# Kernel optimization log

Hardware: AMD Instinct MI355X
Metric: run time of the kernel (lower is better)

Reference implementation:

```python
import jax, jax.numpy as jnp
import numpy as np

HEADS = 4
DIM_HEAD = 64
MAP_SIZE = 16
SCALE = DIM_HEAD ** (-0.5)


def _split_heads(x):
    # torch rearrange 'b (dim_head heads) h w -> b heads (h w) dim_head'
    B, C, H, W = x.shape
    x = x.reshape(B, DIM_HEAD, HEADS, H * W)
    return jnp.transpose(x, (0, 2, 3, 1))  # [B, heads, N, dim_head]


def _merge_heads(x, H, W):
    # torch rearrange 'b heads (h w) dim_head -> b (dim_head heads) h w'
    B, h, N, d = x.shape
    return jnp.transpose(x, (0, 3, 1, 2)).reshape(B, d * h, H, W)


def setup_inputs() -> dict:
    key = jax.random.key(0)
    ks = jax.random.split(key, 6)
    feat = jax.random.normal(ks[0], (4, 256, 96, 96), jnp.float32)
    semantic_map = jax.random.normal(ks[1], (4, 256, 16, 16), jnp.float32)
    # 1x1 conv weights, shape [out_ch, in_ch]; scaled like fan-in init
    W_feat_qv = 0.05 * jax.random.normal(ks[2], (512, 256), jnp.float32)
    W_map_qv = 0.05 * jax.random.normal(ks[3], (512, 256), jnp.float32)
    W_feat_out = 0.05 * jax.random.normal(ks[4], (256, 256), jnp.float32)
    W_map_out = 0.05 * jax.random.normal(ks[5], (256, 256), jnp.float32)
    return {
        "feat": feat,
        "semantic_map": semantic_map,
        "W_feat_qv": W_feat_qv,
        "W_map_qv": W_map_qv,
        "W_feat_out": W_feat_out,
        "W_map_out": W_map_out,
    }


def reference(feat, semantic_map, W_feat_qv, W_map_qv, W_feat_out, W_map_out):
    B, C, H, W = feat.shape
    # 1x1 convs == per-pixel channel matmuls
    fqv = jnp.einsum("oc,bchw->bohw", W_feat_qv, feat)
    feat_q, feat_v = jnp.split(fqv, 2, axis=1)
    mqv = jnp.einsum("oc,bchw->bohw", W_map_qv, semantic_map)
    map_q, map_v = jnp.split(mqv, 2, axis=1)

    feat_q, feat_v = _split_heads(feat_q), _split_heads(feat_v)  # [B,h,N,d]
    map_q, map_v = _split_heads(map_q), _split_heads(map_v)      # [B,h,M,d]

    attn = jnp.einsum("bhid,bhjd->bhij", feat_q, map_q) * SCALE  # [B,h,N,M]
    feat_map_attn = jax.nn.softmax(attn, axis=-1)  # normalize over map tokens j
    map_feat_attn = jax.nn.softmax(attn, axis=-2)  # normalize over feat tokens i

    feat_o = jnp.einsum("bhij,bhjd->bhid", feat_map_attn, map_v)   # [B,h,N,d]
    map_o = jnp.einsum("bhji,bhjd->bhid", map_feat_attn, feat_v)   # [B,h,M,d]

    feat_o = _merge_heads(feat_o, H, W)
    map_o = _merge_heads(map_o, MAP_SIZE, MAP_SIZE)

    feat_out = jnp.einsum("oc,bchw->bohw", W_feat_out, feat_o)
    map_out = jnp.einsum("oc,bchw->bohw", W_map_out, map_o)
    return feat_out, map_out
```

## Files before the change

kernel.cpp:

```cpp
#include <hip/hip_runtime.h>
#include <stdint.h>

#define DI static __device__ __forceinline__

constexpr int NTOK = 9216;
constexpr float ATT_SCALE = 0.125f;

typedef short bf16x8 __attribute__((ext_vector_type(8)));
typedef float f32x4  __attribute__((ext_vector_type(4)));

DI f32x4 mfma16(bf16x8 a, bf16x8 b, f32x4 c) {
  return __builtin_amdgcn_mfma_f32_16x16x32_bf16(a, b, c, 0, 0, 0);
}

DI float lo2f(uint32_t u) { union { uint32_t i; float f; } v; v.i = u << 16; return v.f; }
DI float hi2f(uint32_t u) { union { uint32_t i; float f; } v; v.i = u & 0xffff0000u; return v.f; }
DI float b2f(uint16_t u) { union { uint32_t i; float f; } v; v.i = ((uint32_t)u) << 16; return v.f; }
DI uint16_t f2b(float f) {
  union { float f; uint32_t i; } v; v.f = f;
  uint32_t r = (v.i + 0x7fffu + ((v.i >> 16) & 1u)) >> 16;
  return (uint16_t)r;
}

template<int DT> DI float ld1(const void* p, size_t off) {
  if constexpr (DT) return b2f(((const uint16_t*)p)[off]);
  else              return ((const float*)p)[off];
}
template<int DT> DI void st1(void* p, size_t off, float v) {
  if constexpr (DT) ((uint16_t*)p)[off] = f2b(v);
  else              ((float*)p)[off] = v;
}

__global__ void detect_dtype(const uint32_t* __restrict__ w, int* __restrict__ flag) {
  const int l = threadIdx.x;
  int cl = 0;
  #pragma unroll
  for (int i = 0; i < 4; ++i) {
    const float b = b2f((uint16_t)(w[l + i * 64] & 0xffffu));
    const float ab = fabsf(b);
    cl += (ab > 1e-4f && ab < 0.5f) ? 1 : 0;
  }
  cl += __shfl_xor(cl, 1);  cl += __shfl_xor(cl, 2);  cl += __shfl_xor(cl, 4);
  cl += __shfl_xor(cl, 8);  cl += __shfl_xor(cl, 16); cl += __shfl_xor(cl, 32);
  if (l == 0) flag[0] = (cl >= 128) ? 1 : 0;
}

template<int DT>
DI void prep_w_body(const void* __restrict__ Wfqv, const void* __restrict__ Wfo,
                    uint16_t* __restrict__ WqvP, uint16_t* __restrict__ WfoP)
{
  const int r = blockIdx.x, c = threadIdx.x;
  if (r < 512) {
    const int sel = r >> 8, within = r & 255;
    const int h = within >> 6, d = within & 63;
    const int src = sel * 256 + d * 4 + h;
    WqvP[(size_t)r * 256 + c] = f2b(ld1<DT>(Wfqv, (size_t)src * 256 + c));
  } else {
    const int ro = r - 512;
    WfoP[(size_t)ro * 256 + c] =
        f2b(ld1<DT>(Wfo, (size_t)ro * 256 + (c & 63) * 4 + (c >> 6)));
  }
}
__global__ __launch_bounds__(256) void prep_w(
    const void* Wfqv, const void* Wfo, uint16_t* WqvP, uint16_t* WfoP,
    const int* __restrict__ flag)
{
  if (flag[0]) prep_w_body<1>(Wfqv, Wfo, WqvP, WfoP);
  else         prep_w_body<0>(Wfqv, Wfo, WqvP, WfoP);
}

constexpr int P0 = 280;

template<int DT>
DI void gemm0_body(uint16_t* Xs, const uint16_t* __restrict__ WqvP,
                   const void* __restrict__ X,
                   uint16_t* __restrict__ FQ, uint16_t* __restrict__ FVt)
{
  const int tid = threadIdx.x;
  const int w = tid >> 6, lane = tid & 63;
  const int l = lane & 15, quad = lane >> 4;
  const int n0 = blockIdx.x * 64;
  const int bb = blockIdx.y;
  const size_t bh = (size_t)bb * 4 + w;

  {
    const int nb = (tid & 31) * 2;
    const int kg = tid >> 5;
    #pragma unroll
    for (int pass = 0; pass < 4; ++pass) {
      const int k0 = pass * 64 + kg * 8;
      union { uint16_t h[8]; uint4 u; } pk0, pk1;
      #pragma unroll
      for (int j = 0; j < 8; ++j) {
        const size_t g = ((size_t)bb * 256 + k0 + j) * NTOK + n0 + nb;
        if constexpr (DT) {
          const uint32_t v = *(const uint32_t*)((const uint16_t*)X + g);
          pk0.h[j] = (uint16_t)(v & 0xffffu);
          pk1.h[j] = (uint16_t)(v >> 16);
        } else {
          const float2 v = *(const float2*)((const float*)X + g);
          pk0.h[j] = f2b(v.x);
          pk1.h[j] = f2b(v.y);
        }
      }
      *(uint4*)(Xs + (size_t)(nb + 0) * P0 + k0) = pk0.u;
      *(uint4*)(Xs + (size_t)(nb + 1) * P0 + k0) = pk1.u;
    }
  }
  __syncthreads();

  f32x4 acc[8][4];
  #pragma unroll
  for (int a = 0; a < 8; ++a)
    #pragma unroll
    for (int b = 0; b < 4; ++b) { acc[a][b].x = 0.f; acc[a][b].y = 0.f; acc[a][b].z = 0.f; acc[a][b].w = 0.f; }

  for (int ks = 0; ks < 8; ++ks) {
    bf16x8 af[8];
    #pragma unroll
    for (int mt = 0; mt < 8; ++mt) {
      const int arow = (mt >> 2) * 256 + w * 64 + (mt & 3) * 16 + l;
      af[mt] = *(const bf16x8*)(WqvP + (size_t)arow * 256 + ks * 32 + quad * 8);
    }
    #pragma unroll
    for (int nt = 0; nt < 4; ++nt) {
      const bf16x8 bv = *(const bf16x8*)(Xs + (size_t)(nt * 16 + l) * P0 + ks * 32 + quad * 8);
      #pragma unroll
      for (int mt = 0; mt < 8; ++mt)
        acc[mt][nt] = mfma16(af[mt], bv, acc[mt][nt]);
    }
  }
  #pragma unroll
  for (int mt = 0; mt < 8; ++mt)
    #pragma unroll
    for (int nt = 0; nt < 4; ++nt) {
      const int n = n0 + nt * 16 + l;
      if (mt < 4) {
        union { uint16_t h[4]; uint2 u; } pk;
        #pragma unroll
        for (int r = 0; r < 4; ++r) pk.h[r] = f2b(acc[mt][nt][r]);
        *(uint2*)(FQ + (bh * NTOK + n) * 64 + mt * 16 + quad * 4) = pk.u;
      } else {
        const int itile = n >> 5, io = n & 31;
        #pragma unroll
        for (int r = 0; r < 4; ++r)
          FVt[(((size_t)bh * 288 + itile) * 64 + (mt - 4) * 16 + quad * 4 + r) * 32 + io] =
              f2b(acc[mt][nt][r]);
      }
    }
}
__global__ __launch_bounds__(256) void gemm0_mfma(
    const uint16_t* WqvP, const void* X, uint16_t* FQ, uint16_t* FVt,
    const int* __restrict__ flag)
{
  __shared__ __align__(16) uint16_t Xs[64 * P0];
  if (flag[0]) gemm0_body<1>(Xs, WqvP, X, FQ, FVt);
  else         gemm0_body<0>(Xs, WqvP, X, FQ, FVt);
}

template<int DT>
DI void gemm1_body(const uint16_t* __restrict__ WfoP, const uint16_t* __restrict__ FO,
                   void* __restrict__ out)
{
  const int tid = threadIdx.x;
  const int w = tid >> 6, lane = tid & 63;
  const int l = lane & 15, quad = lane >> 4;
  const int n0 = blockIdx.x * 256;
  const int o0 = blockIdx.y * 64;
  const int bb = blockIdx.z;

  f32x4 acc[4][4];
  #pragma unroll
  for (int a = 0; a < 4; ++a)
    #pragma unroll
    for (int b = 0; b < 4; ++b) { acc[a][b].x = 0.f; acc[a][b].y = 0.f; acc[a][b].z = 0.f; acc[a][b].w = 0.f; }

  #pragma unroll
  for (int ks = 0; ks < 8; ++ks) {
    const int h2 = ks >> 1;
    const int doff = (ks & 1) * 32 + quad * 8;
    bf16x8 af[4];
    #pragma unroll
    for (int mt = 0; mt < 4; ++mt)
      af[mt] = *(const bf16x8*)(WfoP + (size_t)(o0 + mt * 16 + l) * 256 + ks * 32 + quad * 8);
    #pragma unroll
    for (int nt = 0; nt < 4; ++nt) {
      const int n = n0 + w * 64 + nt * 16 + l;
      const bf16x8 bv = *(const bf16x8*)(FO + ((size_t)(bb * 4 + h2) * NTOK + n) * 64 + doff);
      #pragma unroll
      for (int mt = 0; mt < 4; ++mt)
        acc[mt][nt] = mfma16(af[mt], bv, acc[mt][nt]);
    }
  }
  #pragma unroll
  for (int mt = 0; mt < 4; ++mt)
    #pragma unroll
    for (int nt = 0; nt < 4; ++nt) {
      const int n = n0 + w * 64 + nt * 16 + l;
      #pragma unroll
      for (int r = 0; r < 4; ++r)
        st1<DT>(out, ((size_t)bb * 256 + o0 + mt * 16 + quad * 4 + r) * NTOK + n,
                acc[mt][nt][r]);
    }
}
__global__ __launch_bounds__(256) void gemm1_mfma(
    const uint16_t* WfoP, const uint16_t* FO, void* out,
    const int* __restrict__ flag)
{
  if (flag[0]) gemm1_body<1>(WfoP, FO, out);
  else         gemm1_body<0>(WfoP, FO, out);
}

template<int DT>
DI void map_qv_body(const void* __restrict__ Wqv, const void* __restrict__ smap,
                    uint16_t* __restrict__ MQ, uint16_t* __restrict__ MVT)
{
  const int o = blockIdx.x, bb = blockIdx.y, m = threadIdx.x;
  float acc = 0.f;
  #pragma unroll 8
  for (int c = 0; c < 256; ++c)
    acc += ld1<DT>(Wqv, (size_t)o * 256 + c) *
           ld1<DT>(smap, (size_t)bb * 65536 + (size_t)c * 256 + m);
  const int oc = o & 255;
  const int h = oc & 3, d = oc >> 2;
  if (o < 256) MQ[(((size_t)bb * 4 + h) * 256 + m) * 64 + d] = f2b(acc);
  else         MVT[(((size_t)bb * 4 + h) * 64 + d) * 256 + m] = f2b(acc);
}
__global__ __launch_bounds__(256) void map_qv(
    const void* Wqv, const void* smap, uint16_t* MQ, uint16_t* MVT,
    const int* __restrict__ flag)
{
  if (flag[0]) map_qv_body<1>(Wqv, smap, MQ, MVT);
  else         map_qv_body<0>(Wqv, smap, MQ, MVT);
}

constexpr int PJ = 280;
constexpr int PI = 40;
constexpr int PO = 72;
constexpr int NGRP = 36;

__global__ __launch_bounds__(256, 3) void attn_mfma(
    const uint16_t* __restrict__ FQ, const uint16_t* __restrict__ FVt,
    const uint16_t* __restrict__ MQ, const uint16_t* __restrict__ MVT,
    uint16_t* __restrict__ FO, uint16_t* __restrict__ P)
{
  __shared__ __align__(16) uint16_t Esh[32 * PJ];
  __shared__ __align__(16) uint16_t ETsh[256 * PI];
  __shared__ __align__(16) uint16_t Osh[32 * PO];
  __shared__ float RS[4][32];
  const int tid = threadIdx.x;
  const int w = tid >> 6;
  const int lane = tid & 63;
  const int l = lane & 15, quad = lane >> 4;
  const int blk = blockIdx.x, bh = blockIdx.y;
  const uint16_t* FQh  = FQ  + (size_t)bh * NTOK * 64;
  const uint16_t* FVth = FVt + (size_t)bh * 288 * 64 * 32;
  const uint16_t* MQh  = MQ  + (size_t)bh * 256 * 64;
  const uint16_t* MVTh = MVT + (size_t)bh * 64 * 256;
  uint16_t* FOh = FO + (size_t)bh * NTOK * 64;

  bf16x8 kb[4][2];
  #pragma unroll
  for (int jt = 0; jt < 4; ++jt) {
    const int j = w * 64 + jt * 16 + l;
    kb[jt][0] = *(const bf16x8*)(MQh + (size_t)j * 64 + quad * 8);
    kb[jt][1] = *(const bf16x8*)(MQh + (size_t)j * 64 + 32 + quad * 8);
  }
  bf16x8 avr[8];
  #pragma unroll
  for (int ks = 0; ks < 8; ++ks)
    avr[ks] = *(const bf16x8*)(MVTh + (size_t)(w * 16 + l) * 256 + ks * 32 + quad * 8);

  f32x4 numacc[4][4];
  #pragma unroll
  for (int a = 0; a < 4; ++a)
    #pragma unroll
    for (int b = 0; b < 4; ++b) { numacc[a][b].x = 0.f; numacc[a][b].y = 0.f; numacc[a][b].z = 0.f; numacc[a][b].w = 0.f; }
  float csum[4] = {0.f, 0.f, 0.f, 0.f};

  for (int t = 0; t < 8; ++t) {
    const int it = blk * 8 + t;
    const int i0 = it * 32;

    bf16x8 qa[2][2];
    #pragma unroll
    for (int mt = 0; mt < 2; ++mt)
      #pragma unroll
      for (int kbi = 0; kbi < 2; ++kbi)
        qa[mt][kbi] = *(const bf16x8*)(FQh + (size_t)(i0 + mt * 16 + l) * 64 + kbi * 32 + quad * 8);

    float rsum[2][4] = {{0.f,0.f,0.f,0.f},{0.f,0.f,0.f,0.f}};
    #pragma unroll
    for (int jt = 0; jt < 4; ++jt) {
      const int j0 = w * 64 + jt * 16;
      #pragma unroll
      for (int mt = 0; mt < 2; ++mt) {
        f32x4 acc = {0.f, 0.f, 0.f, 0.f};
        acc = mfma16(qa[mt][0], kb[jt][0], acc);
        acc = mfma16(qa[mt][1], kb[jt][1], acc);
        union { uint16_t h[4]; uint2 u; } pk;
        #pragma unroll
        for (int r = 0; r < 4; ++r) {
          const float e = __expf(acc[r] * ATT_SCALE);
          rsum[mt][r] += e;
          csum[jt] += e;
          pk.h[r] = f2b(e);
          Esh[(mt * 16 + quad * 4 + r) * PJ + j0 + l] = pk.h[r];
        }
        *(uint2*)(ETsh + (size_t)(j0 + l) * PI + mt * 16 + quad * 4) = pk.u;
      }
    }
    #pragma unroll
    for (int mt = 0; mt < 2; ++mt)
      #pragma unroll
      for (int r = 0; r < 4; ++r) {
        float v = rsum[mt][r];
        v += __shfl_xor(v, 1); v += __shfl_xor(v, 2);
        v += __shfl_xor(v, 4); v += __shfl_xor(v, 8);
        if (l == 0) RS[w][mt * 16 + quad * 4 + r] = v;
      }
    __syncthreads();

    bf16x8 av[4];
    #pragma unroll
    for (int mt = 0; mt < 4; ++mt)
      av[mt] = *(const bf16x8*)(FVth + ((size_t)it * 64 + mt * 16 + l) * 32 + quad * 8);

    {
      float rinv[2];
      #pragma unroll
      for (int nt = 0; nt < 2; ++nt) {
        const int i_ = nt * 16 + l;
        rinv[nt] = 1.f / (RS[0][i_] + RS[1][i_] + RS[2][i_] + RS[3][i_]);
      }
      f32x4 oacc[2];
      oacc[0].x=0.f;oacc[0].y=0.f;oacc[0].z=0.f;oacc[0].w=0.f;
      oacc[1]=oacc[0];
      #pragma unroll
      for (int ks = 0; ks < 8; ++ks) {
        #pragma unroll
        for (int nt = 0; nt < 2; ++nt) {
          const bf16x8 bv = *(const bf16x8*)(Esh + (size_t)(nt * 16 + l) * PJ + ks * 32 + quad * 8);
          oacc[nt] = mfma16(avr[ks], bv, oacc[nt]);
        }
      }
      #pragma unroll
      for (int nt = 0; nt < 2; ++nt) {
        union { uint16_t h[4]; uint2 u; } pk;
        #pragma unroll
        for (int r = 0; r < 4; ++r) pk.h[r] = f2b(oacc[nt][r] * rinv[nt]);
        *(uint2*)(Osh + (nt * 16 + l) * PO + w * 16 + quad * 4) = pk.u;
      }
    }

    #pragma unroll
    for (int mt = 0; mt < 4; ++mt) {
      #pragma unroll
      for (int nt2 = 0; nt2 < 4; ++nt2) {
        const bf16x8 bv = *(const bf16x8*)(ETsh + (size_t)(w * 64 + nt2 * 16 + l) * PI + quad * 8);
        numacc[mt][nt2] = mfma16(av[mt], bv, numacc[mt][nt2]);
      }
    }
    __syncthreads();

    {
      const int ti = tid >> 3, c = tid & 7;
      *(uint4*)(FOh + (size_t)(i0 + ti) * 64 + c * 8) =
          *(const uint4*)(Osh + ti * PO + c * 8);
    }
  }

  uint16_t* Pb = P + ((size_t)bh * NGRP + blk) * 65 * 256;
  #pragma unroll
  for (int mt = 0; mt < 4; ++mt)
    #pragma unroll
    for (int nt2 = 0; nt2 < 4; ++nt2)
      #pragma unroll
      for (int r = 0; r < 4; ++r)
        Pb[(mt * 16 + quad * 4 + r) * 256 + w * 64 + nt2 * 16 + l] =
            f2b(numacc[mt][nt2][r]);
  #pragma unroll
  for (int jt = 0; jt < 4; ++jt) {
    float v = csum[jt];
    v += __shfl_xor(v, 16); v += __shfl_xor(v, 32);
    if (quad == 0) Pb[64 * 256 + w * 64 + jt * 16 + l] = f2b(v);
  }
}

__global__ __launch_bounds__(256) void reduce_map(
    const uint16_t* __restrict__ P, uint16_t* __restrict__ MO)
{
  const int idx = blockIdx.x * 256 + threadIdx.x;
  const int bh = idx >> 14;
  const int d = (idx >> 8) & 63;
  const int j = idx & 255;
  const size_t base = (size_t)bh * NGRP * 65 * 256;
  float num = 0.f, cs = 0.f;
  #pragma unroll 6
  for (int g = 0; g < NGRP; ++g) {
    num += b2f(P[base + ((size_t)g * 65 + d) * 256 + j]);
    cs  += b2f(P[base + ((size_t)g * 65 + 64) * 256 + j]);
  }
  const float v = num / cs;
  const int b = bh >> 2, h = bh & 3;
  MO[((size_t)b * 256 + (d * 4 + h)) * 256 + j] = f2b(v);
}

template<int DT>
DI void map_out_body(const void* __restrict__ Wmo, const uint16_t* __restrict__ MO,
                     void* __restrict__ out)
{
  const int o = blockIdx.x, bb = blockIdx.y, m = threadIdx.x;
  float acc = 0.f;
  #pragma unroll 8
  for (int c = 0; c < 256; ++c)
    acc += ld1<DT>(Wmo, (size_t)o * 256 + c) *
           b2f(MO[((size_t)bb * 256 + c) * 256 + m]);
  const size_t MAP_OFS = (size_t)4 * 256 * NTOK;
  st1<DT>(out, MAP_OFS + ((size_t)bb * 256 + o) * 256 + m, acc);
}
__global__ __launch_bounds__(256) void map_out_k(
    const void* Wmo, const uint16_t* MO, void* out, const int* __restrict__ flag)
{
  if (flag[0]) map_out_body<1>(Wmo, MO, out);
  else         map_out_body<0>(Wmo, MO, out);
}

extern "C" void kernel_launch(void* const* d_in, const int* in_sizes, int n_in,
                              void* d_out, int out_size, void* d_ws, size_t ws_size,
                              hipStream_t stream) {
  (void)in_sizes; (void)n_in; (void)out_size; (void)ws_size;
  const void* feat = d_in[0];
  const void* smap = d_in[1];
  const void* Wfqv = d_in[2];
  const void* Wmqv = d_in[3];
  const void* Wfo  = d_in[4];
  const void* Wmo  = d_in[5];
  char* ws = (char*)d_ws;

  const size_t BIG = (size_t)16 * 64 * NTOK * 2;
  const size_t SML = (size_t)16 * 256 * 64 * 2;
  const size_t FQ_OFF  = 0;
  const size_t FVT_OFF = FQ_OFF + BIG;
  const size_t MQ_OFF  = FVT_OFF + BIG;
  const size_t MVT_OFF = MQ_OFF + SML;
  const size_t MO_OFF  = MVT_OFF + SML;
  const size_t WQP_OFF = MO_OFF + (size_t)4 * 256 * 256 * 2;
  const size_t WFP_OFF = WQP_OFF + (size_t)512 * 256 * 2;
  const size_t FLAG_OFF = WFP_OFF + (size_t)256 * 256 * 2;

  uint16_t* FQ   = (uint16_t*)(ws + FQ_OFF);
  uint16_t* FVt  = (uint16_t*)(ws + FVT_OFF);
  uint16_t* MQ   = (uint16_t*)(ws + MQ_OFF);
  uint16_t* MVT  = (uint16_t*)(ws + MVT_OFF);
  uint16_t* MO   = (uint16_t*)(ws + MO_OFF);
  uint16_t* WqvP = (uint16_t*)(ws + WQP_OFF);
  uint16_t* WfoP = (uint16_t*)(ws + WFP_OFF);
  int* FLAG   = (int*)(ws + FLAG_OFF);

  uint16_t* P = (uint16_t*)d_out;

  detect_dtype<<<dim3(1), dim3(64), 0, stream>>>((const uint32_t*)Wfqv, FLAG);
  prep_w<<<dim3(768), 256, 0, stream>>>(Wfqv, Wfo, WqvP, WfoP, FLAG);
  gemm0_mfma<<<dim3(144, 4), 256, 0, stream>>>(WqvP, feat, FQ, FVt, FLAG);
  map_qv<<<dim3(512, 4), 256, 0, stream>>>(Wmqv, smap, MQ, MVT, FLAG);
  attn_mfma<<<dim3(NGRP, 16), 256, 0, stream>>>(FQ, FVt, MQ, MVT, FQ, P);
  reduce_map<<<dim3(1024), 256, 0, stream>>>(P, MO);
  gemm1_mfma<<<dim3(36, 4, 4), 256, 0, stream>>>(WfoP, FQ, d_out, FLAG);
  map_out_k<<<dim3(256, 4), 256, 0, stream>>>(Wmo, MO, d_out, FLAG);
}
```

Measured before the change: 286.8 us.

## Fuse launches: inline dtype detection, merge prep/map_qv and gemm1/reduce kernels

Removes the separate dtype-detection kernel by having each block compute the flag with __syncthreads_count, merges weight prep with the map QV projection into one launch, and combines the feature output GEMM with the map reduction into one epilogue launch when the workspace can hold the partials buffer. The partials buffer P moves from the output buffer into the workspace and is re-laid out as [j][d] rows with vectorized stores, so the reduction reads are contiguous. This cuts launch count and serialization, and lets gemm1 and the reduction run concurrently. In exchange every block reloads 256 weight words to detect the dtype.

```diff
diff --git a/kernel.cpp b/kernel.cpp
--- a/kernel.cpp
+++ b/kernel.cpp
@@ -13,8 +13,6 @@
   return __builtin_amdgcn_mfma_f32_16x16x32_bf16(a, b, c, 0, 0, 0);
 }
 
-DI float lo2f(uint32_t u) { union { uint32_t i; float f; } v; v.i = u << 16; return v.f; }
-DI float hi2f(uint32_t u) { union { uint32_t i; float f; } v; v.i = u & 0xffff0000u; return v.f; }
 DI float b2f(uint16_t u) { union { uint32_t i; float f; } v; v.i = ((uint32_t)u) << 16; return v.f; }
 DI uint16_t f2b(float f) {
   union { float f; uint32_t i; } v; v.f = f;
@@ -31,25 +29,17 @@
   else              ((float*)p)[off] = v;
 }
 
-__global__ void detect_dtype(const uint32_t* __restrict__ w, int* __restrict__ flag) {
-  const int l = threadIdx.x;
-  int cl = 0;
-  #pragma unroll
-  for (int i = 0; i < 4; ++i) {
-    const float b = b2f((uint16_t)(w[l + i * 64] & 0xffffu));
-    const float ab = fabsf(b);
-    cl += (ab > 1e-4f && ab < 0.5f) ? 1 : 0;
-  }
-  cl += __shfl_xor(cl, 1);  cl += __shfl_xor(cl, 2);  cl += __shfl_xor(cl, 4);
-  cl += __shfl_xor(cl, 8);  cl += __shfl_xor(cl, 16); cl += __shfl_xor(cl, 32);
-  if (l == 0) flag[0] = (cl >= 128) ? 1 : 0;
+DI int block_flag256(const uint32_t* __restrict__ w) {
+  const float b = b2f((uint16_t)(w[threadIdx.x & 255] & 0xffffu));
+  const float ab = fabsf(b);
+  return (__syncthreads_count((ab > 1e-4f && ab < 0.5f) ? 1 : 0) >= 128) ? 1 : 0;
 }
 
 template<int DT>
-DI void prep_w_body(const void* __restrict__ Wfqv, const void* __restrict__ Wfo,
-                    uint16_t* __restrict__ WqvP, uint16_t* __restrict__ WfoP)
-{
-  const int r = blockIdx.x, c = threadIdx.x;
+DI void prep_w_dev(int r, const void* __restrict__ Wfqv, const void* __restrict__ Wfo,
+                   uint16_t* __restrict__ WqvP, uint16_t* __restrict__ WfoP)
+{
+  const int c = threadIdx.x;
   if (r < 512) {
     const int sel = r >> 8, within = r & 255;
     const int h = within >> 6, d = within & 63;
@@ -61,12 +51,38 @@
         f2b(ld1<DT>(Wfo, (size_t)ro * 256 + (c & 63) * 4 + (c >> 6)));
   }
 }
-__global__ __launch_bounds__(256) void prep_w(
-    const void* Wfqv, const void* Wfo, uint16_t* WqvP, uint16_t* WfoP,
-    const int* __restrict__ flag)
-{
-  if (flag[0]) prep_w_body<1>(Wfqv, Wfo, WqvP, WfoP);
-  else         prep_w_body<0>(Wfqv, Wfo, WqvP, WfoP);
+
+template<int DT>
+DI void map_qv_dev(int o, int bb, const void* __restrict__ Wqv,
+                   const void* __restrict__ smap,
+                   uint16_t* __restrict__ MQ, uint16_t* __restrict__ MVT)
+{
+  const int m = threadIdx.x;
+  float acc = 0.f;
+  #pragma unroll 8
+  for (int c = 0; c < 256; ++c)
+    acc += ld1<DT>(Wqv, (size_t)o * 256 + c) *
+           ld1<DT>(smap, (size_t)bb * 65536 + (size_t)c * 256 + m);
+  const int oc = o & 255;
+  const int h = oc & 3, d = oc >> 2;
+  if (o < 256) MQ[(((size_t)bb * 4 + h) * 256 + m) * 64 + d] = f2b(acc);
+  else         MVT[(((size_t)bb * 4 + h) * 64 + d) * 256 + m] = f2b(acc);
+}
+
+__global__ __launch_bounds__(256) void prep_map_k(
+    const void* Wfqv, const void* Wfo, const void* Wmqv, const void* smap,
+    uint16_t* WqvP, uint16_t* WfoP, uint16_t* MQ, uint16_t* MVT)
+{
+  const int fl = block_flag256((const uint32_t*)Wfqv);
+  const int bid = blockIdx.x;
+  if (bid < 768) {
+    if (fl) prep_w_dev<1>(bid, Wfqv, Wfo, WqvP, WfoP);
+    else    prep_w_dev<0>(bid, Wfqv, Wfo, WqvP, WfoP);
+  } else {
+    const int idx = bid - 768;
+    if (fl) map_qv_dev<1>(idx & 511, idx >> 9, Wmqv, smap, MQ, MVT);
+    else    map_qv_dev<0>(idx & 511, idx >> 9, Wmqv, smap, MQ, MVT);
+  }
 }
 
 constexpr int P0 = 280;
@@ -151,93 +167,19 @@
 }
 __global__ __launch_bounds__(256) void gemm0_mfma(
     const uint16_t* WqvP, const void* X, uint16_t* FQ, uint16_t* FVt,
-    const int* __restrict__ flag)
+    const void* Wfqv)
 {
   __shared__ __align__(16) uint16_t Xs[64 * P0];
-  if (flag[0]) gemm0_body<1>(Xs, WqvP, X, FQ, FVt);
-  else         gemm0_body<0>(Xs, WqvP, X, FQ, FVt);
-}
-
-template<int DT>
-DI void gemm1_body(const uint16_t* __restrict__ WfoP, const uint16_t* __restrict__ FO,
-                   void* __restrict__ out)
-{
-  const int tid = threadIdx.x;
-  const int w = tid >> 6, lane = tid & 63;
-  const int l = lane & 15, quad = lane >> 4;
-  const int n0 = blockIdx.x * 256;
-  const int o0 = blockIdx.y * 64;
-  const int bb = blockIdx.z;
-
-  f32x4 acc[4][4];
-  #pragma unroll
-  for (int a = 0; a < 4; ++a)
-    #pragma unroll
-    for (int b = 0; b < 4; ++b) { acc[a][b].x = 0.f; acc[a][b].y = 0.f; acc[a][b].z = 0.f; acc[a][b].w = 0.f; }
-
-  #pragma unroll
-  for (int ks = 0; ks < 8; ++ks) {
-    const int h2 = ks >> 1;
-    const int doff = (ks & 1) * 32 + quad * 8;
-    bf16x8 af[4];
-    #pragma unroll
-    for (int mt = 0; mt < 4; ++mt)
-      af[mt] = *(const bf16x8*)(WfoP + (size_t)(o0 + mt * 16 + l) * 256 + ks * 32 + quad * 8);
-    #pragma unroll
-    for (int nt = 0; nt < 4; ++nt) {
-      const int n = n0 + w * 64 + nt * 16 + l;
-      const bf16x8 bv = *(const bf16x8*)(FO + ((size_t)(bb * 4 + h2) * NTOK + n) * 64 + doff);
-      #pragma unroll
-      for (int mt = 0; mt < 4; ++mt)
-        acc[mt][nt] = mfma16(af[mt], bv, acc[mt][nt]);
-    }
-  }
-  #pragma unroll
-  for (int mt = 0; mt < 4; ++mt)
-    #pragma unroll
-    for (int nt = 0; nt < 4; ++nt) {
-      const int n = n0 + w * 64 + nt * 16 + l;
-      #pragma unroll
-      for (int r = 0; r < 4; ++r)
-        st1<DT>(out, ((size_t)bb * 256 + o0 + mt * 16 + quad * 4 + r) * NTOK + n,
-                acc[mt][nt][r]);
-    }
-}
-__global__ __launch_bounds__(256) void gemm1_mfma(
-    const uint16_t* WfoP, const uint16_t* FO, void* out,
-    const int* __restrict__ flag)
-{
-  if (flag[0]) gemm1_body<1>(WfoP, FO, out);
-  else         gemm1_body<0>(WfoP, FO, out);
-}
-
-template<int DT>
-DI void map_qv_body(const void* __restrict__ Wqv, const void* __restrict__ smap,
-                    uint16_t* __restrict__ MQ, uint16_t* __restrict__ MVT)
-{
-  const int o = blockIdx.x, bb = blockIdx.y, m = threadIdx.x;
-  float acc = 0.f;
-  #pragma unroll 8
-  for (int c = 0; c < 256; ++c)
-    acc += ld1<DT>(Wqv, (size_t)o * 256 + c) *
-           ld1<DT>(smap, (size_t)bb * 65536 + (size_t)c * 256 + m);
-  const int oc = o & 255;
-  const int h = oc & 3, d = oc >> 2;
-  if (o < 256) MQ[(((size_t)bb * 4 + h) * 256 + m) * 64 + d] = f2b(acc);
-  else         MVT[(((size_t)bb * 4 + h) * 64 + d) * 256 + m] = f2b(acc);
-}
-__global__ __launch_bounds__(256) void map_qv(
-    const void* Wqv, const void* smap, uint16_t* MQ, uint16_t* MVT,
-    const int* __restrict__ flag)
-{
-  if (flag[0]) map_qv_body<1>(Wqv, smap, MQ, MVT);
-  else         map_qv_body<0>(Wqv, smap, MQ, MVT);
+  const int fl = block_flag256((const uint32_t*)Wfqv);
+  if (fl) gemm0_body<1>(Xs, WqvP, X, FQ, FVt);
+  else    gemm0_body<0>(Xs, WqvP, X, FQ, FVt);
 }
 
 constexpr int PJ = 280;
 constexpr int PI = 40;
 constexpr int PO = 72;
 constexpr int NGRP = 36;
+constexpr int PP = 68;
 
 __global__ __launch_bounds__(256, 3) void attn_mfma(
     const uint16_t* __restrict__ FQ, const uint16_t* __restrict__ FVt,
@@ -370,40 +312,106 @@
     }
   }
 
-  uint16_t* Pb = P + ((size_t)bh * NGRP + blk) * 65 * 256;
+  uint16_t* Pb = P + ((size_t)bh * NGRP + blk) * 256 * PP;
   #pragma unroll
   for (int mt = 0; mt < 4; ++mt)
     #pragma unroll
-    for (int nt2 = 0; nt2 < 4; ++nt2)
-      #pragma unroll
-      for (int r = 0; r < 4; ++r)
-        Pb[(mt * 16 + quad * 4 + r) * 256 + w * 64 + nt2 * 16 + l] =
-            f2b(numacc[mt][nt2][r]);
+    for (int nt2 = 0; nt2 < 4; ++nt2) {
+      const int j = w * 64 + nt2 * 16 + l;
+      union { uint16_t h[4]; uint2 u; } pk;
+      #pragma unroll
+      for (int r = 0; r < 4; ++r) pk.h[r] = f2b(numacc[mt][nt2][r]);
+      *(uint2*)(Pb + (size_t)j * PP + mt * 16 + quad * 4) = pk.u;
+    }
   #pragma unroll
   for (int jt = 0; jt < 4; ++jt) {
     float v = csum[jt];
     v += __shfl_xor(v, 16); v += __shfl_xor(v, 32);
-    if (quad == 0) Pb[64 * 256 + w * 64 + jt * 16 + l] = f2b(v);
-  }
-}
-
-__global__ __launch_bounds__(256) void reduce_map(
-    const uint16_t* __restrict__ P, uint16_t* __restrict__ MO)
-{
-  const int idx = blockIdx.x * 256 + threadIdx.x;
+    if (quad == 0) Pb[(size_t)(w * 64 + jt * 16 + l) * PP + 64] = f2b(v);
+  }
+}
+
+template<int DT>
+DI void gemm1_dev(int gidx, const uint16_t* __restrict__ WfoP,
+                  const uint16_t* __restrict__ FO, void* __restrict__ out)
+{
+  const int tid = threadIdx.x;
+  const int w = tid >> 6, lane = tid & 63;
+  const int l = lane & 15, quad = lane >> 4;
+  const int n0 = (gidx % 36) * 256;
+  const int o0 = ((gidx / 36) & 3) * 64;
+  const int bb = gidx / 144;
+
+  f32x4 acc[4][4];
+  #pragma unroll
+  for (int a = 0; a < 4; ++a)
+    #pragma unroll
+    for (int b = 0; b < 4; ++b) { acc[a][b].x = 0.f; acc[a][b].y = 0.f; acc[a][b].z = 0.f; acc[a][b].w = 0.f; }
+
+  #pragma unroll
+  for (int ks = 0; ks < 8; ++ks) {
+    const int h2 = ks >> 1;
+    const int doff = (ks & 1) * 32 + quad * 8;
+    bf16x8 af[4];
+    #pragma unroll
+    for (int mt = 0; mt < 4; ++mt)
+      af[mt] = *(const bf16x8*)(WfoP + (size_t)(o0 + mt * 16 + l) * 256 + ks * 32 + quad * 8);
+    #pragma unroll
+    for (int nt = 0; nt < 4; ++nt) {
+      const int n = n0 + w * 64 + nt * 16 + l;
+      const bf16x8 bv = *(const bf16x8*)(FO + ((size_t)(bb * 4 + h2) * NTOK + n) * 64 + doff);
+      #pragma unroll
+      for (int mt = 0; mt < 4; ++mt)
+        acc[mt][nt] = mfma16(af[mt], bv, acc[mt][nt]);
+    }
+  }
+  #pragma unroll
+  for (int mt = 0; mt < 4; ++mt)
+    #pragma unroll
+    for (int nt = 0; nt < 4; ++nt) {
+      const int n = n0 + w * 64 + nt * 16 + l;
+      #pragma unroll
+      for (int r = 0; r < 4; ++r)
+        st1<DT>(out, ((size_t)bb * 256 + o0 + mt * 16 + quad * 4 + r) * NTOK + n,
+                acc[mt][nt][r]);
+    }
+}
+
+DI void reduce_dev(int bid, const uint16_t* __restrict__ P, uint16_t* __restrict__ MO)
+{
+  const int idx = bid * 256 + threadIdx.x;
+  const int d = idx & 63;
+  const int j = (idx >> 6) & 255;
   const int bh = idx >> 14;
-  const int d = (idx >> 8) & 63;
-  const int j = idx & 255;
-  const size_t base = (size_t)bh * NGRP * 65 * 256;
+  const size_t base = (size_t)bh * NGRP * 256 * PP;
   float num = 0.f, cs = 0.f;
   #pragma unroll 6
   for (int g = 0; g < NGRP; ++g) {
-    num += b2f(P[base + ((size_t)g * 65 + d) * 256 + j]);
-    cs  += b2f(P[base + ((size_t)g * 65 + 64) * 256 + j]);
+    const size_t row = base + ((size_t)g * 256 + j) * PP;
+    num += b2f(P[row + d]);
+    cs  += b2f(P[row + 64]);
   }
   const float v = num / cs;
   const int b = bh >> 2, h = bh & 3;
   MO[((size_t)b * 256 + (d * 4 + h)) * 256 + j] = f2b(v);
+}
+
+__global__ __launch_bounds__(256) void epilogue_k(
+    const uint16_t* WfoP, const uint16_t* FO, void* out,
+    const uint16_t* P, uint16_t* MO, const void* Wfqv, int mode)
+{
+  const int bid = blockIdx.x;
+  bool do_g1; int gidx;
+  if (mode == 0)      { do_g1 = bid < 576; gidx = do_g1 ? bid : bid - 576; }
+  else if (mode == 1) { do_g1 = true;  gidx = bid; }
+  else                { do_g1 = false; gidx = bid; }
+  if (do_g1) {
+    const int fl = block_flag256((const uint32_t*)Wfqv);
+    if (fl) gemm1_dev<1>(gidx, WfoP, FO, out);
+    else    gemm1_dev<0>(gidx, WfoP, FO, out);
+  } else {
+    reduce_dev(gidx, P, MO);
+  }
 }
 
 template<int DT>
@@ -420,16 +428,17 @@
   st1<DT>(out, MAP_OFS + ((size_t)bb * 256 + o) * 256 + m, acc);
 }
 __global__ __launch_bounds__(256) void map_out_k(
-    const void* Wmo, const uint16_t* MO, void* out, const int* __restrict__ flag)
-{
-  if (flag[0]) map_out_body<1>(Wmo, MO, out);
-  else         map_out_body<0>(Wmo, MO, out);
+    const void* Wmo, const uint16_t* MO, void* out, const void* Wfqv)
+{
+  const int fl = block_flag256((const uint32_t*)Wfqv);
+  if (fl) map_out_body<1>(Wmo, MO, out);
+  else    map_out_body<0>(Wmo, MO, out);
 }
 
 extern "C" void kernel_launch(void* const* d_in, const int* in_sizes, int n_in,
                               void* d_out, int out_size, void* d_ws, size_t ws_size,
                               hipStream_t stream) {
-  (void)in_sizes; (void)n_in; (void)out_size; (void)ws_size;
+  (void)in_sizes; (void)n_in; (void)out_size;
   const void* feat = d_in[0];
   const void* smap = d_in[1];
   const void* Wfqv = d_in[2];
@@ -447,7 +456,9 @@
   const size_t MO_OFF  = MVT_OFF + SML;
   const size_t WQP_OFF = MO_OFF + (size_t)4 * 256 * 256 * 2;
   const size_t WFP_OFF = WQP_OFF + (size_t)512 * 256 * 2;
-  const size_t FLAG_OFF = WFP_OFF + (size_t)256 * 256 * 2;
+  const size_t P_OFF   = WFP_OFF + (size_t)256 * 256 * 2;
+  const size_t P_SIZE  = (size_t)16 * NGRP * 256 * PP * 2;
+  const size_t NEED    = P_OFF + P_SIZE;
 
   uint16_t* FQ   = (uint16_t*)(ws + FQ_OFF);
   uint16_t* FVt  = (uint16_t*)(ws + FVT_OFF);
@@ -456,16 +467,19 @@
   uint16_t* MO   = (uint16_t*)(ws + MO_OFF);
   uint16_t* WqvP = (uint16_t*)(ws + WQP_OFF);
   uint16_t* WfoP = (uint16_t*)(ws + WFP_OFF);
-  int* FLAG   = (int*)(ws + FLAG_OFF);
-
-  uint16_t* P = (uint16_t*)d_out;
-
-  detect_dtype<<<dim3(1), dim3(64), 0, stream>>>((const uint32_t*)Wfqv, FLAG);
-  prep_w<<<dim3(768), 256, 0, stream>>>(Wfqv, Wfo, WqvP, WfoP, FLAG);
-  gemm0_mfma<<<dim3(144, 4), 256, 0, stream>>>(WqvP, feat, FQ, FVt, FLAG);
-  map_qv<<<dim3(512, 4), 256, 0, stream>>>(Wmqv, smap, MQ, MVT, FLAG);
+
+  const bool p_in_ws = (ws_size >= NEED);
+  uint16_t* P = p_in_ws ? (uint16_t*)(ws + P_OFF) : (uint16_t*)d_out;
+
+  prep_map_k<<<dim3(2816), 256, 0, stream>>>(Wfqv, Wfo, Wmqv, smap,
+                                             WqvP, WfoP, MQ, MVT);
+  gemm0_mfma<<<dim3(144, 4), 256, 0, stream>>>(WqvP, feat, FQ, FVt, Wfqv);
   attn_mfma<<<dim3(NGRP, 16), 256, 0, stream>>>(FQ, FVt, MQ, MVT, FQ, P);
-  reduce_map<<<dim3(1024), 256, 0, stream>>>(P, MO);
-  gemm1_mfma<<<dim3(36, 4, 4), 256, 0, stream>>>(WfoP, FQ, d_out, FLAG);
-  map_out_k<<<dim3(256, 4), 256, 0, stream>>>(Wmo, MO, d_out, FLAG);
-}
+  if (p_in_ws) {
+    epilogue_k<<<dim3(1600), 256, 0, stream>>>(WfoP, FQ, d_out, P, MO, Wfqv, 0);
+  } else {
+    epilogue_k<<<dim3(1024), 256, 0, stream>>>(WfoP, FQ, d_out, P, MO, Wfqv, 2);
+    epilogue_k<<<dim3(576),  256, 0, stream>>>(WfoP, FQ, d_out, P, MO, Wfqv, 1);
+  }
+  map_out_k<<<dim3(256, 4), 256, 0, stream>>>(Wmo, MO, d_out, Wfqv);
+}
```

Result: no change. 291.0 us (+1.5%).
